# Kernel tuning notes

Hardware: AMD Instinct MI355X
Metric: run time of the kernel (lower is better)

## Reference

```python
import jax, jax.numpy as jnp
import numpy as np

D_MODEL = 1024
NHEAD = 16
HEAD_DIM = D_MODEL // NHEAD
DIM_FF = 4096
B, TC, TP = 4, 1024, 1024
EPS = 1e-5


def _layernorm(x, g, b):
    mu = jnp.mean(x, axis=-1, keepdims=True)
    var = jnp.mean(jnp.square(x - mu), axis=-1, keepdims=True)
    return (x - mu) * jax.lax.rsqrt(var + EPS) * g + b


def setup_inputs() -> dict:
    key = jax.random.key(0)
    ks = jax.random.split(key, 12)
    s = 0.02
    return {
        "x": jax.random.normal(ks[0], (B, TC, D_MODEL), jnp.float32),
        "Kp": jax.random.normal(ks[1], (B, NHEAD, TP, HEAD_DIM), jnp.float32),
        "Vp": jax.random.normal(ks[2], (B, NHEAD, TP, HEAD_DIM), jnp.float32),
        "pos_offset": TP,
        "wqkv": jax.random.normal(ks[3], (D_MODEL, 3 * D_MODEL), jnp.float32) * s,
        "bqkv": jnp.zeros((3 * D_MODEL,), jnp.float32),
        "wo": jax.random.normal(ks[4], (D_MODEL, D_MODEL), jnp.float32) * s,
        "bo": jnp.zeros((D_MODEL,), jnp.float32),
        "g1": jnp.ones((D_MODEL,), jnp.float32),
        "be1": jnp.zeros((D_MODEL,), jnp.float32),
        "g2": jnp.ones((D_MODEL,), jnp.float32),
        "be2": jnp.zeros((D_MODEL,), jnp.float32),
        "w1": jax.random.normal(ks[5], (D_MODEL, DIM_FF), jnp.float32) * s,
        "bf1": jnp.zeros((DIM_FF,), jnp.float32),
        "w2": jax.random.normal(ks[6], (DIM_FF, D_MODEL), jnp.float32) * s,
        "bf2": jnp.zeros((D_MODEL,), jnp.float32),
    }


def reference(x, Kp, Vp, pos_offset, wqkv, bqkv, wo, bo, g1, be1, g2, be2, w1, bf1, w2, bf2):
    Bsz, Tc, D = x.shape
    H, Dh = NHEAD, HEAD_DIM
    h = _layernorm(x, g1, be1)
    qkv = (h @ wqkv + bqkv).reshape(Bsz, Tc, 3, H, Dh).transpose(2, 0, 3, 1, 4)
    q, k_new, v_new = qkv[0], qkv[1], qkv[2]  # [B,H,Tc,Dh]
    K = jnp.concatenate([Kp, k_new], axis=2)  # [B,H,Tk,Dh]
    V = jnp.concatenate([Vp, v_new], axis=2)
    Tk = K.shape[2]
    scale = Dh ** -0.5
    # fused causal-masked attention; equivalent to the per-token loop:
    # query i attends keys j with j <= pos_offset + i
    scores = jnp.einsum("bhqd,bhkd->bhqk", q, K) * scale
    q_idx = jnp.arange(Tc)[:, None]
    k_idx = jnp.arange(Tk)[None, :]
    mask = k_idx <= (pos_offset + q_idx)  # [Tc,Tk]
    scores = jnp.where(mask, scores, jnp.finfo(scores.dtype).min)
    attn = jax.nn.softmax(scores, axis=-1)
    o = jnp.einsum("bhqk,bhkd->bhqd", attn, V)
    o = o.transpose(0, 2, 1, 3).reshape(Bsz, Tc, D)
    x = x + o @ wo + bo
    h2 = _layernorm(x, g2, be2)
    ff = jax.nn.gelu(h2 @ w1 + bf1, approximate=False) @ w2 + bf2
    x = x + ff
    return x, K, V
```

## Files before the change

kernel.cpp:

```cpp
#include <hip/hip_runtime.h>
#include <math.h>

#define DM   1024
#define NH   16
#define DH   64
#define DFF  4096
#define BSZ  4
#define TCC  1024
#define TPP  1024
#define TKK  2048
#define NTOK (BSZ*TCC)

typedef __attribute__((ext_vector_type(8))) short bf16x8;
typedef __attribute__((ext_vector_type(4))) float f32x4;

__device__ __forceinline__ unsigned short f2bf(float x) {
  union { float f; unsigned u; } v; v.f = x;
  unsigned r = v.u + 0x7fffu + ((v.u >> 16) & 1u);
  return (unsigned short)(r >> 16);
}
__device__ __forceinline__ unsigned pk2(float a, float b) {
  return (unsigned)f2bf(a) | ((unsigned)f2bf(b) << 16);
}

__device__ __forceinline__ void gload16(const void* g, void* l) {
  __builtin_amdgcn_global_load_lds(
      (const __attribute__((address_space(1))) void*)g,
      (__attribute__((address_space(3))) void*)l, 16, 0, 0);
}

__device__ __forceinline__ float wave_reduce_sum(float v) {
#pragma unroll
  for (int off = 32; off > 0; off >>= 1)
    v += __shfl_down(v, off, 64);
  return v;
}

__device__ __forceinline__ float gelu_f(float x) {
  float z = fabsf(x) * 0.70710678118654752440f;
  float t = 1.0f / (1.0f + 0.3275911f * z);
  float y = t * (0.254829592f +
            t * (-0.284496736f +
            t * (1.421413741f +
            t * (-1.453152027f +
            t * 1.061405429f))));
  float e = __expf(-z * z);
  float erfz = 1.0f - y * e;
  float s = (x >= 0.0f) ? erfz : -erfz;
  return 0.5f * x * (1.0f + s);
}

__global__ __launch_bounds__(256) void castT_kernel(
    const float* __restrict__ W, unsigned short* __restrict__ Wt, int K, int N) {
  __shared__ float tile[32][33];
  int nb = blockIdx.x << 5, kb = blockIdx.y << 5;
  int c = threadIdx.x & 31, r8 = threadIdx.x >> 5;
#pragma unroll
  for (int i = 0; i < 32; i += 8)
    tile[r8 + i][c] = W[(size_t)(kb + r8 + i) * N + nb + c];
  __syncthreads();
#pragma unroll
  for (int i = 0; i < 32; i += 8)
    Wt[(size_t)(nb + r8 + i) * K + kb + c] = f2bf(tile[c][r8 + i]);
}

__global__ __launch_bounds__(256) void castVt_kernel(
    const float* __restrict__ V, unsigned short* __restrict__ Vt) {
  __shared__ float tile[32][33];
  int z = blockIdx.z;
  const float* W = V + (size_t)z * TKK * DH;
  unsigned short* Wt = Vt + (size_t)z * DH * TKK;
  int nb = blockIdx.x << 5;
  int kb = blockIdx.y << 5;
  int c = threadIdx.x & 31, r8 = threadIdx.x >> 5;
#pragma unroll
  for (int i = 0; i < 32; i += 8)
    tile[r8 + i][c] = W[(size_t)(kb + r8 + i) * DH + nb + c];
  __syncthreads();
#pragma unroll
  for (int i = 0; i < 32; i += 8)
    Wt[(size_t)(nb + r8 + i) * TKK + kb + c] = f2bf(tile[c][r8 + i]);
}

__global__ __launch_bounds__(256) void copy_kv_kernel(
    const float4* __restrict__ Kp, const float4* __restrict__ Vp,
    float4* __restrict__ Kout, float4* __restrict__ Vout,
    unsigned short* __restrict__ Kbf) {
  int idx = blockIdx.x * 256 + threadIdx.x;
  int r = idx >> 4;
  int c = idx & 15;
  int dr = (r >> 10) * TKK + (r & 1023);
  float4 kv = Kp[idx];
  Kout[dr * 16 + c] = kv;
  Vout[dr * 16 + c] = Vp[idx];
  if (Kbf != nullptr) {
    uint2 pk;
    pk.x = pk2(kv.x, kv.y);
    pk.y = pk2(kv.z, kv.w);
    *(uint2*)(Kbf + (size_t)(dr * 16 + c) * 4) = pk;
  }
}

__global__ __launch_bounds__(256) void ln_kernel(
    const float* __restrict__ x, const float* __restrict__ g,
    const float* __restrict__ b, unsigned short* __restrict__ out) {
  __shared__ float red[8];
  int row = blockIdx.x;
  int tid = threadIdx.x;
  const float4* xr = (const float4*)(x + (size_t)row * DM);
  float4 xv = xr[tid];
  float s  = xv.x + xv.y + xv.z + xv.w;
  float ss = xv.x*xv.x + xv.y*xv.y + xv.z*xv.z + xv.w*xv.w;
  s  = wave_reduce_sum(s);
  ss = wave_reduce_sum(ss);
  int lane = tid & 63, wid = tid >> 6;
  if (lane == 0) { red[wid] = s; red[4 + wid] = ss; }
  __syncthreads();
  s  = red[0] + red[1] + red[2] + red[3];
  ss = red[4] + red[5] + red[6] + red[7];
  float mu  = s * (1.0f / DM);
  float var = ss * (1.0f / DM) - mu * mu;
  float rs  = rsqrtf(var + 1e-5f);
  float4 gv = ((const float4*)g)[tid];
  float4 bv = ((const float4*)b)[tid];
  ushort4 ov;
  ov.x = f2bf((xv.x - mu) * rs * gv.x + bv.x);
  ov.y = f2bf((xv.y - mu) * rs * gv.y + bv.y);
  ov.z = f2bf((xv.z - mu) * rs * gv.z + bv.z);
  ov.w = f2bf((xv.w - mu) * rs * gv.w + bv.w);
  *(ushort4*)&out[(size_t)row * DM + tid * 4] = ov;
}

__global__ __launch_bounds__(256) void reduce2_kernel(
    float* __restrict__ xout, const float* __restrict__ bf2,
    const float* __restrict__ pA, const float* __restrict__ pB) {
  int idx = blockIdx.x * 256 + threadIdx.x;
  float4 o = ((const float4*)xout)[idx];
  float4 b = ((const float4*)bf2)[idx & 255];
  float4 a = ((const float4*)pA)[idx];
  float4 c = ((const float4*)pB)[idx];
  o.x += b.x + a.x + c.x;
  o.y += b.y + a.y + c.y;
  o.z += b.z + a.z + c.z;
  o.w += b.w + a.w + c.w;
  ((float4*)xout)[idx] = o;
}

template <int MODE, int NSPLIT>
__global__ __launch_bounds__(512) void mm8_kernel(
    const unsigned short* __restrict__ A, const unsigned short* __restrict__ Bt,
    const float* __restrict__ bias, const float* __restrict__ res,
    float* __restrict__ outf, unsigned short* __restrict__ outb,
    float* __restrict__ Kc, float* __restrict__ Vc,
    unsigned short* __restrict__ Kbfp,
    int M, int N, int K) {
  __shared__ __align__(16) short lds[4][2][8192];
  int tid = threadIdx.x;
  int l = tid & 63, w = tid >> 6;
  int wr = w >> 2, wc = w & 3;
  int cidx = l & 15, rg = l >> 4;
  int m0 = blockIdx.y << 8, n0 = blockIdx.x << 8;
  int z = (NSPLIT > 1) ? blockIdx.z : 0;
  int KS = K / NSPLIT;

  int r0 = tid >> 2;
  int cb = (((tid & 3) ^ ((r0 >> 1) & 3)) << 4);
  const char* gA = (const char*)A + (size_t)(m0 + r0) * 2 * K + cb + (size_t)2 * z * KS;
  const char* gB = (const char*)Bt + (size_t)(n0 + r0) * 2 * K + cb + (size_t)2 * z * KS;
  size_t rskip = (size_t)128 * 2 * K;

  int xcs = ((rg ^ ((cidx >> 1) & 3)) << 4);
  int offA = (wr * 128 + cidx) * 64 + xcs;
  int offB = (wc * 64 + cidx) * 64 + xcs;

  f32x4 acc[8][4] = {};
  int NT = KS >> 5;

  auto stage = [&](int t, int half) {
    char* la = (char*)&lds[t & 3][0][0] + tid * 16 + half * 8192;
    char* lb = (char*)&lds[t & 3][1][0] + tid * 16 + half * 8192;
    const char* sa = gA + t * 64 + (half ? rskip : 0);
    const char* sb = gB + t * 64 + (half ? rskip : 0);
    gload16(sa, la);
    gload16(sb, lb);
  };

  stage(0, 0); stage(0, 1);
  stage(1, 0); stage(1, 1);
  stage(2, 0); stage(2, 1);
  asm volatile("s_waitcnt vmcnt(8)" ::: "memory");
  __builtin_amdgcn_sched_barrier(0);
  __builtin_amdgcn_s_barrier();

  for (int t = 0; t < NT; ++t) {
    const char* pa = (const char*)&lds[t & 3][0][0];
    const char* pb = (const char*)&lds[t & 3][1][0];
    bf16x8 af[4], bg[4], a2[4];
#pragma unroll
    for (int i = 0; i < 4; ++i)
      af[i] = *(const bf16x8*)(pa + offA + i * 1024);
#pragma unroll
    for (int j = 0; j < 4; ++j)
      bg[j] = *(const bf16x8*)(pb + offB + j * 1024);
    if (t + 3 < NT) stage(t + 3, 0);
    __builtin_amdgcn_s_barrier();
    asm volatile("s_waitcnt lgkmcnt(0)" ::: "memory");
    __builtin_amdgcn_sched_barrier(0);
    __builtin_amdgcn_s_setprio(1);
#pragma unroll
    for (int i = 0; i < 4; ++i)
#pragma unroll
      for (int j = 0; j < 4; ++j)
        acc[i][j] = __builtin_amdgcn_mfma_f32_16x16x32_bf16(
            af[i], bg[j], acc[i][j], 0, 0, 0);
    __builtin_amdgcn_s_setprio(0);
    __builtin_amdgcn_s_barrier();
#pragma unroll
    for (int i = 0; i < 4; ++i)
      a2[i] = *(const bf16x8*)(pa + offA + (i + 4) * 1024);
    if (t + 3 < NT) stage(t + 3, 1);
    if (t + 3 < NT) {
      asm volatile("s_waitcnt vmcnt(8)" ::: "memory");
    } else if (t + 2 < NT) {
      asm volatile("s_waitcnt vmcnt(4)" ::: "memory");
    } else {
      asm volatile("s_waitcnt vmcnt(0)" ::: "memory");
    }
    __builtin_amdgcn_sched_barrier(0);
    __builtin_amdgcn_s_barrier();
    asm volatile("s_waitcnt lgkmcnt(0)" ::: "memory");
    __builtin_amdgcn_sched_barrier(0);
    __builtin_amdgcn_s_setprio(1);
#pragma unroll
    for (int i = 0; i < 4; ++i)
#pragma unroll
      for (int j = 0; j < 4; ++j)
        acc[i + 4][j] = __builtin_amdgcn_mfma_f32_16x16x32_bf16(
            a2[i], bg[j], acc[i + 4][j], 0, 0, 0);
    __builtin_amdgcn_s_setprio(0);
    __builtin_amdgcn_s_barrier();
  }

#pragma unroll
  for (int i = 0; i < 8; ++i) {
#pragma unroll
    for (int j = 0; j < 4; ++j) {
      int col = n0 + wc * 64 + j * 16 + cidx;
      float bb = bias[col];
#pragma unroll
      for (int r = 0; r < 4; ++r) {
        int row = m0 + wr * 128 + i * 16 + rg * 4 + r;
        float v = acc[i][j][r] + bb;
        if (MODE == 0) {
          int which = col >> 10, c = col & 1023;
          int hh = c >> 6, dd = c & 63;
          int b = row >> 10, tt = row & 1023;
          size_t base = (size_t)(b * NH + hh);
          if (which == 0)      outb[(base * TCC + tt) * DH + dd] = f2bf(v * 0.125f);
          else if (which == 1) {
            size_t off = (base * TKK + TPP + tt) * DH + dd;
            Kc[off] = v;
            if (Kbfp != nullptr) Kbfp[off] = f2bf(v);
          } else               Vc[(base * TKK + TPP + tt) * DH + dd] = v;
        } else if (MODE == 2) {
          outb[(size_t)row * N + col] = f2bf(gelu_f(v));
        } else {
          float* dst = (z == 0) ? outf : Kc;
          dst[(size_t)row * N + col] = acc[i][j][r];
        }
      }
    }
  }
}

template <int MODE, int DEPTH>
__global__ __launch_bounds__(256) void mm_kernel(
    const unsigned short* __restrict__ A, const unsigned short* __restrict__ Bt,
    const float* __restrict__ bias, const float* __restrict__ res,
    float* __restrict__ outf, unsigned short* __restrict__ outb,
    int M, int N, int K) {
  __shared__ __align__(16) short As[DEPTH * 128 * 32];
  __shared__ __align__(16) short Bs[DEPTH * 128 * 32];
  int tid = threadIdx.x;
  int w = tid >> 6, l = tid & 63;
  int m0 = blockIdx.y << 7, n0 = blockIdx.x << 7;
  int wm = (w >> 1) << 6, wn = (w & 1) << 6;
  int cidx = l & 15, rg = l >> 4;
  f32x4 acc[4][4] = {};

  int idx0 = w * 1024 + l * 16;
  int idx1 = idx0 + 4096;
  const char* gA0 = (const char*)A + (size_t)(m0 + (idx0 >> 6)) * 2 * K + (idx0 & 63);
  const char* gA1 = (const char*)A + (size_t)(m0 + (idx1 >> 6)) * 2 * K + (idx1 & 63);
  const char* gB0 = (const char*)Bt + (size_t)(n0 + (idx0 >> 6)) * 2 * K + (idx0 & 63);
  const char* gB1 = (const char*)Bt + (size_t)(n0 + (idx1 >> 6)) * 2 * K + (idx1 & 63);

  auto stage = [&](int bsel) {
    char* base_a = (char*)As + bsel * 8192;
    char* base_b = (char*)Bs + bsel * 8192;
    gload16(gA0, base_a + idx0); gload16(gA1, base_a + idx1);
    gload16(gB0, base_b + idx0); gload16(gB1, base_b + idx1);
    gA0 += 64; gA1 += 64; gB0 += 64; gB1 += 64;
  };
  auto compute = [&](int bsel) {
    const short* pa = As + bsel * 4096;
    const short* pb = Bs + bsel * 4096;
    bf16x8 af[4], bfr[4];
#pragma unroll
    for (int i = 0; i < 4; ++i) {
      af[i]  = *(const bf16x8*)&pa[(wm + i * 16 + cidx) * 32 + rg * 8];
      bfr[i] = *(const bf16x8*)&pb[(wn + i * 16 + cidx) * 32 + rg * 8];
    }
#pragma unroll
    for (int i = 0; i < 4; ++i)
#pragma unroll
      for (int j = 0; j < 4; ++j)
        acc[i][j] = __builtin_amdgcn_mfma_f32_16x16x32_bf16(
            af[i], bfr[j], acc[i][j], 0, 0, 0);
  };

  int nt = K >> 5;
  stage(0); stage(1); stage(2);
  for (int t = 0; t < nt - 3; ++t) {
    asm volatile("s_waitcnt vmcnt(8)" ::: "memory");
    __builtin_amdgcn_sched_barrier(0);
    __builtin_amdgcn_s_barrier();
    __builtin_amdgcn_sched_barrier(0);
    stage((t + 3) & 3);
    compute(t & 3);
  }
  asm volatile("s_waitcnt vmcnt(8)" ::: "memory");
  __builtin_amdgcn_sched_barrier(0);
  __builtin_amdgcn_s_barrier();
  __builtin_amdgcn_sched_barrier(0);
  compute((nt - 3) & 3);
  asm volatile("s_waitcnt vmcnt(4)" ::: "memory");
  __builtin_amdgcn_sched_barrier(0);
  __builtin_amdgcn_s_barrier();
  __builtin_amdgcn_sched_barrier(0);
  compute((nt - 2) & 3);
  asm volatile("s_waitcnt vmcnt(0)" ::: "memory");
  __builtin_amdgcn_sched_barrier(0);
  __builtin_amdgcn_s_barrier();
  __builtin_amdgcn_sched_barrier(0);
  compute((nt - 1) & 3);

#pragma unroll
  for (int i = 0; i < 4; ++i) {
#pragma unroll
    for (int j = 0; j < 4; ++j) {
      int col = n0 + wn + j * 16 + cidx;
      float bb = bias[col];
#pragma unroll
      for (int r = 0; r < 4; ++r) {
        int row = m0 + wm + i * 16 + rg * 4 + r;
        float v = acc[i][j][r] + bb;
        size_t off = (size_t)row * N + col;
        outf[off] = res[off] + v;
      }
    }
  }
}

template <int KBF>
__global__ __launch_bounds__(256) void attn_kernel(
    const unsigned short* __restrict__ Qb, const float* __restrict__ K,
    const unsigned short* __restrict__ Kb16,
    const unsigned short* __restrict__ Vtb, const int* __restrict__ posp,
    unsigned short* __restrict__ o) {
  __shared__ __align__(16) unsigned short Qs[64][72];
  __shared__ __align__(16) unsigned short Ks[64][72];
  __shared__ __align__(16) unsigned short Vts[64][72];
  __shared__ __align__(16) unsigned short Pw[4][16][72];
  int tid = threadIdx.x;
  int w = tid >> 6, lane = tid & 63;
  int l15 = lane & 15, quad = lane >> 4;
  int blk = blockIdx.x;
  int bh = blk >> 4;
  int qbase = (blk & 15) << 6;
  int b = bh >> 4, h = bh & 15;
  int pos = *posp;

  {
    int r = tid >> 2, cg = (tid & 3) << 4;
    const unsigned short* src = Qb + ((size_t)bh * TCC + qbase + r) * DH + cg;
    *(uint4*)&Qs[r][cg]     = *(const uint4*)src;
    *(uint4*)&Qs[r][cg + 8] = *(const uint4*)(src + 8);
  }
  __syncthreads();
  bf16x8 aq0 = *(const bf16x8*)&Qs[16 * w + l15][quad * 8];
  bf16x8 aq1 = *(const bf16x8*)&Qs[16 * w + l15][32 + quad * 8];

  f32x4 accO[4] = {};
  f32x4 accL = {};
  bf16x8 ones;
#pragma unroll
  for (int i = 0; i < 8; ++i) ones[i] = (short)0x3F80;

  int nk = pos + qbase + 64; if (nk > TKK) nk = TKK;
  int ntiles = nk >> 6;
  const float* Kbh = K + (size_t)bh * TKK * DH;
  const unsigned short* Kbh16 = Kb16 + (size_t)bh * TKK * DH;
  const unsigned short* Vbh = Vtb + (size_t)bh * DH * TKK;

  for (int t = 0; t < ntiles; ++t) {
    int kt = t << 6;
    {
      int r = tid >> 2, cg = (tid & 3) << 4;
      if (KBF) {
        const unsigned short* ks = Kbh16 + (size_t)(kt + r) * DH + cg;
        *(uint4*)&Ks[r][cg]     = *(const uint4*)ks;
        *(uint4*)&Ks[r][cg + 8] = *(const uint4*)(ks + 8);
      } else {
        const float* ks = Kbh + (size_t)(kt + r) * DH + cg;
        float4 k0 = *(const float4*)ks,       k1 = *(const float4*)(ks + 4);
        float4 k2 = *(const float4*)(ks + 8), k3 = *(const float4*)(ks + 12);
        uint4 p0, p1;
        p0.x = pk2(k0.x, k0.y); p0.y = pk2(k0.z, k0.w);
        p0.z = pk2(k1.x, k1.y); p0.w = pk2(k1.z, k1.w);
        p1.x = pk2(k2.x, k2.y); p1.y = pk2(k2.z, k2.w);
        p1.z = pk2(k3.x, k3.y); p1.w = pk2(k3.z, k3.w);
        *(uint4*)&Ks[r][cg]     = p0;
        *(uint4*)&Ks[r][cg + 8] = p1;
      }
      const unsigned short* vs = Vbh + (size_t)r * TKK + kt + cg;
      *(uint4*)&Vts[r][cg]     = *(const uint4*)vs;
      *(uint4*)&Vts[r][cg + 8] = *(const uint4*)(vs + 8);
    }
    __syncthreads();
    f32x4 accS[4] = {};
    __builtin_amdgcn_s_setprio(1);
#pragma unroll
    for (int j = 0; j < 4; ++j) {
      bf16x8 bk0 = *(const bf16x8*)&Ks[16 * j + l15][quad * 8];
      bf16x8 bk1 = *(const bf16x8*)&Ks[16 * j + l15][32 + quad * 8];
      accS[j] = __builtin_amdgcn_mfma_f32_16x16x32_bf16(aq0, bk0, accS[j], 0, 0, 0);
      accS[j] = __builtin_amdgcn_mfma_f32_16x16x32_bf16(aq1, bk1, accS[j], 0, 0, 0);
    }
    __builtin_amdgcn_s_setprio(0);
    bool edge = (kt + 63 > pos + qbase);
#pragma unroll
    for (int j = 0; j < 4; ++j) {
      int key = kt + 16 * j + l15;
#pragma unroll
      for (int r = 0; r < 4; ++r) {
        float p = __expf(accS[j][r]);
        if (edge && key > pos + qbase + 16 * w + quad * 4 + r) p = 0.f;
        Pw[w][quad * 4 + r][16 * j + l15] = f2bf(p);
      }
    }
    bf16x8 ap0 = *(const bf16x8*)&Pw[w][l15][quad * 8];
    bf16x8 ap1 = *(const bf16x8*)&Pw[w][l15][32 + quad * 8];
    __builtin_amdgcn_s_setprio(1);
    accL = __builtin_amdgcn_mfma_f32_16x16x32_bf16(ap0, ones, accL, 0, 0, 0);
    accL = __builtin_amdgcn_mfma_f32_16x16x32_bf16(ap1, ones, accL, 0, 0, 0);
#pragma unroll
    for (int j2 = 0; j2 < 4; ++j2) {
      bf16x8 bv0 = *(const bf16x8*)&Vts[16 * j2 + l15][quad * 8];
      bf16x8 bv1 = *(const bf16x8*)&Vts[16 * j2 + l15][32 + quad * 8];
      accO[j2] = __builtin_amdgcn_mfma_f32_16x16x32_bf16(ap0, bv0, accO[j2], 0, 0, 0);
      accO[j2] = __builtin_amdgcn_mfma_f32_16x16x32_bf16(ap1, bv1, accO[j2], 0, 0, 0);
    }
    __builtin_amdgcn_s_setprio(0);
    __syncthreads();
  }
#pragma unroll
  for (int r = 0; r < 4; ++r) {
    float inv = 1.0f / accL[r];
    int qg = qbase + 16 * w + quad * 4 + r;
    size_t base = (((size_t)(b * TCC + qg)) * NH + h) * DH;
#pragma unroll
    for (int j2 = 0; j2 < 4; ++j2)
      o[base + 16 * j2 + l15] = f2bf(accO[j2][r] * inv);
  }
}

extern "C" void kernel_launch(void* const* d_in, const int* in_sizes, int n_in,
                              void* d_out, int out_size, void* d_ws, size_t ws_size,
                              hipStream_t stream) {
  (void)in_sizes; (void)n_in; (void)out_size;
  const float* x    = (const float*)d_in[0];
  const float* Kp   = (const float*)d_in[1];
  const float* Vp   = (const float*)d_in[2];
  const int*   posp = (const int*)d_in[3];
  const float* wqkv = (const float*)d_in[4];
  const float* bqkv = (const float*)d_in[5];
  const float* wo   = (const float*)d_in[6];
  const float* bo   = (const float*)d_in[7];
  const float* g1   = (const float*)d_in[8];
  const float* be1  = (const float*)d_in[9];
  const float* g2   = (const float*)d_in[10];
  const float* be2  = (const float*)d_in[11];
  const float* w1   = (const float*)d_in[12];
  const float* bf1  = (const float*)d_in[13];
  const float* w2   = (const float*)d_in[14];
  const float* bf2  = (const float*)d_in[15];

  float* xout = (float*)d_out;
  float* Kout = xout + (size_t)BSZ * TCC * DM;
  float* Vout = Kout + (size_t)BSZ * NH * TKK * DH;

  const size_t MB = 1024 * 1024;
  char* ws = (char*)d_ws;
  unsigned short* wqkvT = (unsigned short*)(ws);
  unsigned short* woT   = (unsigned short*)(ws + 6 * MB);
  unsigned short* w1T   = (unsigned short*)(ws + 8 * MB);
  unsigned short* w2T   = (unsigned short*)(ws + 16 * MB);
  unsigned short* hbf   = (unsigned short*)(ws + 24 * MB);
  unsigned short* ffbf  = (unsigned short*)(ws + 32 * MB);
  unsigned short* Qbuf  = (unsigned short*)(ws + 32 * MB);
  unsigned short* obf   = (unsigned short*)(ws + 40 * MB);
  unsigned short* Vtb   = (unsigned short*)(ws + 48 * MB);
  float*          x2    = xout;
  bool big = (ws_size >= 80 * MB);
  unsigned short* Kbf = big ? (unsigned short*)(ws + 64 * MB) : nullptr;
  float* pfA = (float*)(ws);
  float* pfB = (float*)(ws + 64 * MB);

  castT_kernel<<<dim3(96, 32),  dim3(256), 0, stream>>>(wqkv, wqkvT, DM, 3 * DM);
  castT_kernel<<<dim3(32, 32),  dim3(256), 0, stream>>>(wo,   woT,   DM, DM);
  castT_kernel<<<dim3(128, 32), dim3(256), 0, stream>>>(w1,   w1T,   DM, DFF);
  castT_kernel<<<dim3(32, 128), dim3(256), 0, stream>>>(w2,   w2T,   DFF, DM);

  copy_kv_kernel<<<dim3(4096), dim3(256), 0, stream>>>(
      (const float4*)Kp, (const float4*)Vp, (float4*)Kout, (float4*)Vout, Kbf);
  ln_kernel<<<dim3(NTOK), dim3(256), 0, stream>>>(x, g1, be1, hbf);
  mm8_kernel<0, 1><<<dim3(12, 16), dim3(512), 0, stream>>>(
      hbf, wqkvT, bqkv, nullptr, nullptr, Qbuf, Kout, Vout, Kbf, NTOK, 3 * DM, DM);
  castVt_kernel<<<dim3(2, 64, 64), dim3(256), 0, stream>>>(Vout, Vtb);
  if (Kbf != nullptr)
    attn_kernel<1><<<dim3(1024), dim3(256), 0, stream>>>(Qbuf, Kout, Kbf, Vtb, posp, obf);
  else
    attn_kernel<0><<<dim3(1024), dim3(256), 0, stream>>>(Qbuf, Kout, Kbf, Vtb, posp, obf);
  mm_kernel<1, 4><<<dim3(8, 32), dim3(256), 0, stream>>>(
      obf, woT, bo, x, x2, nullptr, NTOK, DM, DM);
  ln_kernel<<<dim3(NTOK), dim3(256), 0, stream>>>(x2, g2, be2, hbf);
  mm8_kernel<2, 1><<<dim3(16, 16), dim3(512), 0, stream>>>(
      hbf, w1T, bf1, nullptr, nullptr, ffbf, nullptr, nullptr, nullptr, NTOK, DFF, DM);
  if (big) {
    mm8_kernel<4, 2><<<dim3(4, 16, 2), dim3(512), 0, stream>>>(
        ffbf, w2T, bf2, nullptr, pfA, nullptr, pfB, nullptr, nullptr, NTOK, DM, DFF);
    reduce2_kernel<<<dim3(4096), dim3(256), 0, stream>>>(xout, bf2, pfA, pfB);
  } else {
    mm_kernel<1, 4><<<dim3(8, 32), dim3(256), 0, stream>>>(
        ffbf, w2T, bf2, x2, xout, nullptr, NTOK, DM, DFF);
  }
}
```

Measured before the change: 471.3 us.

## Add 128-query attention kernel with direct-to-LDS swizzled K/V loads

Adds attn2_kernel, which processes 128 queries per block with 8 waves, so each K/V tile loaded into shared memory is reused by twice as many queries. K/V tiles are loaded with a gload16 helper (likely global-to-LDS) into an XOR-swizzled layout to avoid bank conflicts. Waves whose queries are fully masked for a tile skip that tile's MFMA work. The cost is a larger block, half as many blocks, and a causal load imbalance across waves inside a block. The fallback kernel also loses its bf16-K variant and its setprio hints.

After: 525.3 us. +11.5%, slower.

```diff
diff --git a/kernel.cpp b/kernel.cpp
--- a/kernel.cpp
+++ b/kernel.cpp
@@ -362,10 +362,111 @@
   }
 }
 
-template <int KBF>
+__global__ __launch_bounds__(512) void attn2_kernel(
+    const unsigned short* __restrict__ Qb,
+    const unsigned short* __restrict__ Kb16,
+    const unsigned short* __restrict__ Vtb, const int* __restrict__ posp,
+    unsigned short* __restrict__ o) {
+  __shared__ __align__(16) unsigned short Qs[128][72];
+  __shared__ __align__(16) unsigned short Ks[64 * 64];
+  __shared__ __align__(16) unsigned short Vts[64 * 64];
+  __shared__ __align__(16) unsigned short Pw[8][16][72];
+  int tid = threadIdx.x;
+  int w = tid >> 6, lane = tid & 63;
+  int l15 = lane & 15, quad = lane >> 4;
+  int blk = blockIdx.x;
+  int bh = blk & 63;
+  int qbase = (blk >> 6) << 7;
+  int b = bh >> 4, h = bh & 15;
+  int pos = *posp;
+
+  {
+    int r = tid >> 2, cg = (tid & 3) << 4;
+    const unsigned short* src = Qb + ((size_t)bh * TCC + qbase + r) * DH + cg;
+    *(uint4*)&Qs[r][cg]     = *(const uint4*)src;
+    *(uint4*)&Qs[r][cg + 8] = *(const uint4*)(src + 8);
+  }
+  __syncthreads();
+  bf16x8 aq0 = *(const bf16x8*)&Qs[16 * w + l15][quad * 8];
+  bf16x8 aq1 = *(const bf16x8*)&Qs[16 * w + l15][32 + quad * 8];
+
+  f32x4 accO[4] = {};
+  f32x4 accL = {};
+  bf16x8 ones;
+#pragma unroll
+  for (int i = 0; i < 8; ++i) ones[i] = (short)0x3F80;
+
+  int srow = tid >> 3;
+  int scolb = (tid & 7) << 4;
+  int scolbx = scolb ^ ((srow & 7) << 4);
+  const char* gK = (const char*)(Kb16 + (size_t)bh * TKK * DH) + scolbx;
+  const char* gV = (const char*)(Vtb + ((size_t)bh * DH + srow) * TKK) + scolbx;
+  char* lK = (char*)Ks + tid * 16;
+  char* lV = (char*)Vts + tid * 16;
+  int rsw = (l15 & 7) << 4;
+
+  int nk = pos + qbase + 128; if (nk > TKK) nk = TKK;
+  int ntiles = nk >> 6;
+  int qwl = pos + qbase + 16 * w;
+
+  for (int t = 0; t < ntiles; ++t) {
+    int kt = t << 6;
+    gload16(gK + (size_t)(kt + srow) * 128, lK);
+    gload16(gV + (size_t)kt * 2, lV);
+    __syncthreads();
+    if (kt <= qwl + 15) {
+      f32x4 accS[4] = {};
+      __builtin_amdgcn_s_setprio(1);
+#pragma unroll
+      for (int j = 0; j < 4; ++j) {
+        const char* kr = (const char*)Ks + (16 * j + l15) * 128;
+        bf16x8 bk0 = *(const bf16x8*)(kr + ((quad * 16) ^ rsw));
+        bf16x8 bk1 = *(const bf16x8*)(kr + ((64 + quad * 16) ^ rsw));
+        accS[j] = __builtin_amdgcn_mfma_f32_16x16x32_bf16(aq0, bk0, accS[j], 0, 0, 0);
+        accS[j] = __builtin_amdgcn_mfma_f32_16x16x32_bf16(aq1, bk1, accS[j], 0, 0, 0);
+      }
+      __builtin_amdgcn_s_setprio(0);
+      bool edge = (kt + 63 > qwl);
+#pragma unroll
+      for (int j = 0; j < 4; ++j) {
+        int key = kt + 16 * j + l15;
+#pragma unroll
+        for (int r = 0; r < 4; ++r) {
+          float p = __expf(accS[j][r]);
+          if (edge && key > qwl + quad * 4 + r) p = 0.f;
+          Pw[w][quad * 4 + r][16 * j + l15] = f2bf(p);
+        }
+      }
+      bf16x8 ap0 = *(const bf16x8*)&Pw[w][l15][quad * 8];
+      bf16x8 ap1 = *(const bf16x8*)&Pw[w][l15][32 + quad * 8];
+      __builtin_amdgcn_s_setprio(1);
+      accL = __builtin_amdgcn_mfma_f32_16x16x32_bf16(ap0, ones, accL, 0, 0, 0);
+      accL = __builtin_amdgcn_mfma_f32_16x16x32_bf16(ap1, ones, accL, 0, 0, 0);
+#pragma unroll
+      for (int j2 = 0; j2 < 4; ++j2) {
+        const char* vr = (const char*)Vts + (16 * j2 + l15) * 128;
+        bf16x8 bv0 = *(const bf16x8*)(vr + ((quad * 16) ^ rsw));
+        bf16x8 bv1 = *(const bf16x8*)(vr + ((64 + quad * 16) ^ rsw));
+        accO[j2] = __builtin_amdgcn_mfma_f32_16x16x32_bf16(ap0, bv0, accO[j2], 0, 0, 0);
+        accO[j2] = __builtin_amdgcn_mfma_f32_16x16x32_bf16(ap1, bv1, accO[j2], 0, 0, 0);
+      }
+      __builtin_amdgcn_s_setprio(0);
+    }
+    __syncthreads();
+  }
+#pragma unroll
+  for (int r = 0; r < 4; ++r) {
+    float inv = 1.0f / accL[r];
+    int qg = qbase + 16 * w + quad * 4 + r;
+    size_t base = (((size_t)(b * TCC + qg)) * NH + h) * DH;
+#pragma unroll
+    for (int j2 = 0; j2 < 4; ++j2)
+      o[base + 16 * j2 + l15] = f2bf(accO[j2][r] * inv);
+  }
+}
+
 __global__ __launch_bounds__(256) void attn_kernel(
     const unsigned short* __restrict__ Qb, const float* __restrict__ K,
-    const unsigned short* __restrict__ Kb16,
     const unsigned short* __restrict__ Vtb, const int* __restrict__ posp,
     unsigned short* __restrict__ o) {
   __shared__ __align__(16) unsigned short Qs[64][72];
@@ -380,7 +481,6 @@
   int qbase = (blk & 15) << 6;
   int b = bh >> 4, h = bh & 15;
   int pos = *posp;
-
   {
     int r = tid >> 2, cg = (tid & 3) << 4;
     const unsigned short* src = Qb + ((size_t)bh * TCC + qbase + r) * DH + cg;
@@ -390,46 +490,35 @@
   __syncthreads();
   bf16x8 aq0 = *(const bf16x8*)&Qs[16 * w + l15][quad * 8];
   bf16x8 aq1 = *(const bf16x8*)&Qs[16 * w + l15][32 + quad * 8];
-
   f32x4 accO[4] = {};
   f32x4 accL = {};
   bf16x8 ones;
 #pragma unroll
   for (int i = 0; i < 8; ++i) ones[i] = (short)0x3F80;
-
   int nk = pos + qbase + 64; if (nk > TKK) nk = TKK;
   int ntiles = nk >> 6;
   const float* Kbh = K + (size_t)bh * TKK * DH;
-  const unsigned short* Kbh16 = Kb16 + (size_t)bh * TKK * DH;
   const unsigned short* Vbh = Vtb + (size_t)bh * DH * TKK;
-
   for (int t = 0; t < ntiles; ++t) {
     int kt = t << 6;
     {
       int r = tid >> 2, cg = (tid & 3) << 4;
-      if (KBF) {
-        const unsigned short* ks = Kbh16 + (size_t)(kt + r) * DH + cg;
-        *(uint4*)&Ks[r][cg]     = *(const uint4*)ks;
-        *(uint4*)&Ks[r][cg + 8] = *(const uint4*)(ks + 8);
-      } else {
-        const float* ks = Kbh + (size_t)(kt + r) * DH + cg;
-        float4 k0 = *(const float4*)ks,       k1 = *(const float4*)(ks + 4);
-        float4 k2 = *(const float4*)(ks + 8), k3 = *(const float4*)(ks + 12);
-        uint4 p0, p1;
-        p0.x = pk2(k0.x, k0.y); p0.y = pk2(k0.z, k0.w);
-        p0.z = pk2(k1.x, k1.y); p0.w = pk2(k1.z, k1.w);
-        p1.x = pk2(k2.x, k2.y); p1.y = pk2(k2.z, k2.w);
-        p1.z = pk2(k3.x, k3.y); p1.w = pk2(k3.z, k3.w);
-        *(uint4*)&Ks[r][cg]     = p0;
-        *(uint4*)&Ks[r][cg + 8] = p1;
-      }
+      const float* ks = Kbh + (size_t)(kt + r) * DH + cg;
+      float4 k0 = *(const float4*)ks,       k1 = *(const float4*)(ks + 4);
+      float4 k2 = *(const float4*)(ks + 8), k3 = *(const float4*)(ks + 12);
+      uint4 p0, p1;
+      p0.x = pk2(k0.x, k0.y); p0.y = pk2(k0.z, k0.w);
+      p0.z = pk2(k1.x, k1.y); p0.w = pk2(k1.z, k1.w);
+      p1.x = pk2(k2.x, k2.y); p1.y = pk2(k2.z, k2.w);
+      p1.z = pk2(k3.x, k3.y); p1.w = pk2(k3.z, k3.w);
+      *(uint4*)&Ks[r][cg]     = p0;
+      *(uint4*)&Ks[r][cg + 8] = p1;
       const unsigned short* vs = Vbh + (size_t)r * TKK + kt + cg;
       *(uint4*)&Vts[r][cg]     = *(const uint4*)vs;
       *(uint4*)&Vts[r][cg + 8] = *(const uint4*)(vs + 8);
     }
     __syncthreads();
     f32x4 accS[4] = {};
-    __builtin_amdgcn_s_setprio(1);
 #pragma unroll
     for (int j = 0; j < 4; ++j) {
       bf16x8 bk0 = *(const bf16x8*)&Ks[16 * j + l15][quad * 8];
@@ -437,7 +526,6 @@
       accS[j] = __builtin_amdgcn_mfma_f32_16x16x32_bf16(aq0, bk0, accS[j], 0, 0, 0);
       accS[j] = __builtin_amdgcn_mfma_f32_16x16x32_bf16(aq1, bk1, accS[j], 0, 0, 0);
     }
-    __builtin_amdgcn_s_setprio(0);
     bool edge = (kt + 63 > pos + qbase);
 #pragma unroll
     for (int j = 0; j < 4; ++j) {
@@ -451,7 +539,6 @@
     }
     bf16x8 ap0 = *(const bf16x8*)&Pw[w][l15][quad * 8];
     bf16x8 ap1 = *(const bf16x8*)&Pw[w][l15][32 + quad * 8];
-    __builtin_amdgcn_s_setprio(1);
     accL = __builtin_amdgcn_mfma_f32_16x16x32_bf16(ap0, ones, accL, 0, 0, 0);
     accL = __builtin_amdgcn_mfma_f32_16x16x32_bf16(ap1, ones, accL, 0, 0, 0);
 #pragma unroll
@@ -461,7 +548,6 @@
       accO[j2] = __builtin_amdgcn_mfma_f32_16x16x32_bf16(ap0, bv0, accO[j2], 0, 0, 0);
       accO[j2] = __builtin_amdgcn_mfma_f32_16x16x32_bf16(ap1, bv1, accO[j2], 0, 0, 0);
     }
-    __builtin_amdgcn_s_setprio(0);
     __syncthreads();
   }
 #pragma unroll
@@ -528,10 +614,10 @@
   mm8_kernel<0, 1><<<dim3(12, 16), dim3(512), 0, stream>>>(
       hbf, wqkvT, bqkv, nullptr, nullptr, Qbuf, Kout, Vout, Kbf, NTOK, 3 * DM, DM);
   castVt_kernel<<<dim3(2, 64, 64), dim3(256), 0, stream>>>(Vout, Vtb);
-  if (Kbf != nullptr)
-    attn_kernel<1><<<dim3(1024), dim3(256), 0, stream>>>(Qbuf, Kout, Kbf, Vtb, posp, obf);
+  if (big)
+    attn2_kernel<<<dim3(512), dim3(512), 0, stream>>>(Qbuf, Kbf, Vtb, posp, obf);
   else
-    attn_kernel<0><<<dim3(1024), dim3(256), 0, stream>>>(Qbuf, Kout, Kbf, Vtb, posp, obf);
+    attn_kernel<<<dim3(1024), dim3(256), 0, stream>>>(Qbuf, Kout, Vtb, posp, obf);
   mm_kernel<1, 4><<<dim3(8, 32), dim3(256), 0, stream>>>(
       obf, woT, bo, x, x2, nullptr, NTOK, DM, DM);
   ln_kernel<<<dim3(NTOK), dim3(256), 0, stream>>>(x2, g2, be2, hbf);
```
